# Kernel tuning notes

Measured on AMD Instinct MI355X. Metric: run time of the kernel, lower is better.

The kernel has to match this reference:

```python
import jax, jax.numpy as jnp
import numpy as np
from jax.ops import segment_sum

N_NODES = 50000
N_EDGES = 800000
HIDDEN = 96
N_CLASSES = 10
N_GRAPHS = 64


def gcn_conv(x, W, b, src, dst, num_nodes):
    """PyG GCNConv: symmetric-normalized aggregation with self-loops.
    out = D^{-1/2} (A + I) D^{-1/2} (x W) + b, with D the degree of A + I.
    Self-loop contribution handled analytically instead of appending edges.
    """
    ones = jnp.ones((src.shape[0],), dtype=x.dtype)
    deg = segment_sum(ones, dst, num_segments=num_nodes) + 1.0  # +1 for self-loop
    dinv = jax.lax.rsqrt(deg)
    h = x @ W  # [N, H] small GEMM
    norm = dinv[src] * dinv[dst]  # [E]
    msg = h[src] * norm[:, None]  # [E, H] dominant gather
    out = segment_sum(msg, dst, num_segments=num_nodes)  # scatter-add
    out = out + h * (dinv * dinv)[:, None]  # self-loop term
    return out + b


def setup_inputs() -> dict:
    key = jax.random.key(0)
    ks = jax.random.split(key, 12)
    x = jax.random.normal(ks[0], (N_NODES, HIDDEN), dtype=jnp.float32)
    edge_index = jax.random.randint(ks[1], (2, N_EDGES), 0, N_NODES, dtype=jnp.int64)
    batch = jnp.sort(jax.random.randint(ks[2], (N_NODES,), 0, N_GRAPHS, dtype=jnp.int64))
    s = 1.0 / np.sqrt(HIDDEN)
    W0 = jax.random.normal(ks[3], (HIDDEN, HIDDEN), dtype=jnp.float32) * s
    b0 = jnp.zeros((HIDDEN,), dtype=jnp.float32)
    W1 = jax.random.normal(ks[4], (HIDDEN, HIDDEN), dtype=jnp.float32) * s
    b1 = jnp.zeros((HIDDEN,), dtype=jnp.float32)
    W2 = jax.random.normal(ks[5], (HIDDEN, HIDDEN), dtype=jnp.float32) * s
    b2 = jnp.zeros((HIDDEN,), dtype=jnp.float32)
    W_lin = jax.random.normal(ks[6], (HIDDEN, N_CLASSES), dtype=jnp.float32) * s
    b_lin = jnp.zeros((N_CLASSES,), dtype=jnp.float32)
    return {"x": x, "edge_index": edge_index, "batch": batch,
            "W0": W0, "b0": b0, "W1": W1, "b1": b1, "W2": W2, "b2": b2,
            "W_lin": W_lin, "b_lin": b_lin}


def reference(x, edge_index, batch, W0, b0, W1, b1, W2, b2, W_lin, b_lin):
    src, dst = edge_index[0], edge_index[1]
    n = x.shape[0]
    h = jax.nn.relu(gcn_conv(x, W0, b0, src, dst, n))
    h = jax.nn.relu(gcn_conv(h, W1, b1, src, dst, n))
    h = gcn_conv(h, W2, b2, src, dst, n)  # last layer: no activation
    # global_mean_pool over batch index
    sums = segment_sum(h, batch, num_segments=N_GRAPHS)  # [G, H]
    cnts = segment_sum(jnp.ones((n,), dtype=h.dtype), batch, num_segments=N_GRAPHS)
    pooled = sums / jnp.maximum(cnts, 1.0)[:, None]
    # dropout is identity in eval mode
    return pooled @ W_lin + b_lin  # [G, num_classes]
```

## Files before the change

kernel.cpp:

```cpp
#include <hip/hip_runtime.h>
#include <hip/hip_bf16.h>

#define HID 96
#define NGRAPHS 64
#define SENT 0xC3C3u
#define NROWS 50116

typedef __attribute__((ext_vector_type(8))) short short8;
typedef __attribute__((ext_vector_type(4))) float floatx4;
typedef __attribute__((ext_vector_type(8))) unsigned short ushort8v;

__device__ __forceinline__ float bf16_to_f32(unsigned short u) {
    unsigned int v = ((unsigned int)u) << 16;
    return __builtin_bit_cast(float, v);
}
__device__ __forceinline__ unsigned short f32_to_bf16(float f) {
    unsigned int u = __builtin_bit_cast(unsigned int, f);
    u += 0x7fff + ((u >> 16) & 1);
    return (unsigned short)(u >> 16);
}

__device__ __forceinline__ void gather_batch(const unsigned short* __restrict__ h,
                                             const unsigned short* __restrict__ csr,
                                             int i, int fi, float& a0, float& a1) {
    ushort8v iv = *(const ushort8v*)(csr + i);
    ushort2 v0 = *(const ushort2*)(h + (size_t)iv[0] * HID + fi);
    ushort2 v1 = *(const ushort2*)(h + (size_t)iv[1] * HID + fi);
    ushort2 v2 = *(const ushort2*)(h + (size_t)iv[2] * HID + fi);
    ushort2 v3 = *(const ushort2*)(h + (size_t)iv[3] * HID + fi);
    ushort2 v4 = *(const ushort2*)(h + (size_t)iv[4] * HID + fi);
    ushort2 v5 = *(const ushort2*)(h + (size_t)iv[5] * HID + fi);
    ushort2 v6 = *(const ushort2*)(h + (size_t)iv[6] * HID + fi);
    ushort2 v7 = *(const ushort2*)(h + (size_t)iv[7] * HID + fi);
    a0 += bf16_to_f32(v0.x) + bf16_to_f32(v1.x) + bf16_to_f32(v2.x) +
          bf16_to_f32(v3.x) + bf16_to_f32(v4.x) + bf16_to_f32(v5.x) +
          bf16_to_f32(v6.x) + bf16_to_f32(v7.x);
    a1 += bf16_to_f32(v0.y) + bf16_to_f32(v1.y) + bf16_to_f32(v2.y) +
          bf16_to_f32(v3.y) + bf16_to_f32(v4.y) + bf16_to_f32(v5.y) +
          bf16_to_f32(v6.y) + bf16_to_f32(v7.y);
}

__device__ __forceinline__ void gather2(const unsigned short* __restrict__ h,
                                        const unsigned short* __restrict__ csr,
                                        int i0, int e0, int i1, int e1, int fi,
                                        float& a00, float& a01, float& a10,
                                        float& a11) {
    ushort8v ivA, ivB;
    if (i0 < e0) ivA = *(const ushort8v*)(csr + i0);
    if (i1 < e1) ivB = *(const ushort8v*)(csr + i1);
    while (i0 < e0 && i1 < e1) {
        ushort8v ca = ivA, cb = ivB;
        i0 += 8;
        i1 += 8;
        if (i0 < e0) ivA = *(const ushort8v*)(csr + i0);
        if (i1 < e1) ivB = *(const ushort8v*)(csr + i1);
        ushort2 u0 = *(const ushort2*)(h + (size_t)ca[0] * HID + fi);
        ushort2 u1 = *(const ushort2*)(h + (size_t)ca[1] * HID + fi);
        ushort2 u2 = *(const ushort2*)(h + (size_t)ca[2] * HID + fi);
        ushort2 u3 = *(const ushort2*)(h + (size_t)ca[3] * HID + fi);
        ushort2 u4 = *(const ushort2*)(h + (size_t)ca[4] * HID + fi);
        ushort2 u5 = *(const ushort2*)(h + (size_t)ca[5] * HID + fi);
        ushort2 u6 = *(const ushort2*)(h + (size_t)ca[6] * HID + fi);
        ushort2 u7 = *(const ushort2*)(h + (size_t)ca[7] * HID + fi);
        ushort2 w0 = *(const ushort2*)(h + (size_t)cb[0] * HID + fi);
        ushort2 w1 = *(const ushort2*)(h + (size_t)cb[1] * HID + fi);
        ushort2 w2 = *(const ushort2*)(h + (size_t)cb[2] * HID + fi);
        ushort2 w3 = *(const ushort2*)(h + (size_t)cb[3] * HID + fi);
        ushort2 w4 = *(const ushort2*)(h + (size_t)cb[4] * HID + fi);
        ushort2 w5 = *(const ushort2*)(h + (size_t)cb[5] * HID + fi);
        ushort2 w6 = *(const ushort2*)(h + (size_t)cb[6] * HID + fi);
        ushort2 w7 = *(const ushort2*)(h + (size_t)cb[7] * HID + fi);
        a00 += bf16_to_f32(u0.x) + bf16_to_f32(u1.x) + bf16_to_f32(u2.x) +
               bf16_to_f32(u3.x) + bf16_to_f32(u4.x) + bf16_to_f32(u5.x) +
               bf16_to_f32(u6.x) + bf16_to_f32(u7.x);
        a01 += bf16_to_f32(u0.y) + bf16_to_f32(u1.y) + bf16_to_f32(u2.y) +
               bf16_to_f32(u3.y) + bf16_to_f32(u4.y) + bf16_to_f32(u5.y) +
               bf16_to_f32(u6.y) + bf16_to_f32(u7.y);
        a10 += bf16_to_f32(w0.x) + bf16_to_f32(w1.x) + bf16_to_f32(w2.x) +
               bf16_to_f32(w3.x) + bf16_to_f32(w4.x) + bf16_to_f32(w5.x) +
               bf16_to_f32(w6.x) + bf16_to_f32(w7.x);
        a11 += bf16_to_f32(w0.y) + bf16_to_f32(w1.y) + bf16_to_f32(w2.y) +
               bf16_to_f32(w3.y) + bf16_to_f32(w4.y) + bf16_to_f32(w5.y) +
               bf16_to_f32(w6.y) + bf16_to_f32(w7.y);
    }
    for (; i0 < e0; i0 += 8) gather_batch(h, csr, i0, fi, a00, a01);
    for (; i1 < e1; i1 += 8) gather_batch(h, csr, i1, fi, a10, a11);
}

__global__ void deg_kernel(const int* __restrict__ dst, int* __restrict__ deg,
                           int n_edges) {
    int t = blockIdx.x * blockDim.x + threadIdx.x;
    int e0 = t * 4;
    if (e0 + 4 <= n_edges) {
        int4 d4 = *(const int4*)(dst + e0);
        atomicAdd(&deg[d4.x], 1);
        atomicAdd(&deg[d4.y], 1);
        atomicAdd(&deg[d4.z], 1);
        atomicAdd(&deg[d4.w], 1);
    } else {
        for (int e = e0; e < n_edges; e++) atomicAdd(&deg[dst[e]], 1);
    }
}

__global__ __launch_bounds__(256) void scan_phaseA(const int* __restrict__ deg,
                                                   float* __restrict__ dinv,
                                                   int* __restrict__ blocksum,
                                                   int N) {
    int i = blockIdx.x * 256 + threadIdx.x;
    int d = (i < N) ? deg[i] : 0;
    if (i < N) dinv[i] = rsqrtf((float)d + 1.0f);
    int v = (d + 7) & ~7;
#pragma unroll
    for (int off = 32; off > 0; off >>= 1) v += __shfl_down(v, off, 64);
    __shared__ int s[4];
    if ((threadIdx.x & 63) == 0) s[threadIdx.x >> 6] = v;
    __syncthreads();
    if (threadIdx.x == 0) blocksum[blockIdx.x] = s[0] + s[1] + s[2] + s[3];
}

__global__ __launch_bounds__(256) void scan_phaseB(int* __restrict__ blocksum,
                                                   int* __restrict__ blockoff,
                                                   int nblocks) {
    __shared__ int s[256];
    int t = threadIdx.x;
    int own = (t < nblocks) ? blocksum[t] : 0;
    s[t] = own;
    __syncthreads();
#pragma unroll
    for (int off = 1; off < 256; off <<= 1) {
        int v = (t >= off) ? s[t - off] : 0;
        __syncthreads();
        s[t] += v;
        __syncthreads();
    }
    if (t < nblocks) blockoff[t] = s[t] - own;
}

__global__ __launch_bounds__(256) void scan_phaseC(const int* __restrict__ deg,
                                                   const int* __restrict__ blockoff,
                                                   int* __restrict__ rowptr,
                                                   int* __restrict__ cursor, int N) {
    __shared__ int s[256];
    int t = threadIdx.x;
    int i = blockIdx.x * 256 + t;
    int own = (i < N) ? (deg[i] + 7) & ~7 : 0;
    s[t] = own;
    __syncthreads();
#pragma unroll
    for (int off = 1; off < 256; off <<= 1) {
        int v = (t >= off) ? s[t - off] : 0;
        __syncthreads();
        s[t] += v;
        __syncthreads();
    }
    if (i < N) {
        int r = blockoff[blockIdx.x] + s[t] - own;
        rowptr[i] = r;
        cursor[i] = r;
        if (i == N - 1) rowptr[N] = r + own;
    }
}

__global__ void csr_fill(const int* __restrict__ src, const int* __restrict__ dst,
                         int* __restrict__ cursor,
                         unsigned short* __restrict__ csr_src, int n_edges) {
    int t = blockIdx.x * blockDim.x + threadIdx.x;
    int e0 = t * 4;
    if (e0 + 4 <= n_edges) {
        int4 d4 = *(const int4*)(dst + e0);
        int4 s4 = *(const int4*)(src + e0);
        int p0 = atomicAdd(&cursor[d4.x], 1);
        int p1 = atomicAdd(&cursor[d4.y], 1);
        int p2 = atomicAdd(&cursor[d4.z], 1);
        int p3 = atomicAdd(&cursor[d4.w], 1);
        csr_src[p0] = (unsigned short)s4.x;
        csr_src[p1] = (unsigned short)s4.y;
        csr_src[p2] = (unsigned short)s4.z;
        csr_src[p3] = (unsigned short)s4.w;
    } else {
        for (int e = e0; e < n_edges; e++) {
            int p = atomicAdd(&cursor[dst[e]], 1);
            csr_src[p] = (unsigned short)src[e];
        }
    }
}

__global__ void swizzle_W(const float* __restrict__ W0, const float* __restrict__ W1,
                          const float* __restrict__ W2, unsigned short* __restrict__ Wz) {
    const float* W = (blockIdx.x == 0) ? W0 : (blockIdx.x == 1) ? W1 : W2;
    unsigned short* dst = Wz + blockIdx.x * HID * HID;
    for (int e = threadIdx.x; e < HID * HID; e += blockDim.x) {
        int k = e / HID, n = e % HID;
        int nt = n >> 4, kki = k >> 5, quad = (k >> 3) & 3, j = k & 7;
        int lane = (n & 15) | (quad << 4);
        dst[(((nt * 3 + kki) * 64 + lane) << 3) | j] = f32_to_bf16(W[e]);
    }
}

__global__ void zero_sentinel(unsigned short* __restrict__ a,
                              unsigned short* __restrict__ b) {
    int t = threadIdx.x;
    a[(size_t)SENT * HID + t] = 0;
    b[(size_t)SENT * HID + t] = 0;
}

__global__ __launch_bounds__(256) void gemm0_f32(
    const float* __restrict__ X, const unsigned short* __restrict__ Wz,
    const float* __restrict__ dinv, unsigned short* __restrict__ Out, int Mtiles) {
    int wv = threadIdx.x >> 6;
    int lane = threadIdx.x & 63;
    int quad = lane >> 4;
    int mrow = lane & 15;
    int tt = blockIdx.x * 2 + (wv >> 1);
    int half = wv & 1;
    if (tt >= Mtiles) return;

    short8 bfrag[9];
    const short8* Wz8 = (const short8*)Wz;
#pragma unroll
    for (int f = 0; f < 9; f++) bfrag[f] = Wz8[(half * 9 + f) * 64 + lane];

    int m0 = tt * 16;
    const float* arow = X + (size_t)(m0 + mrow) * HID + quad * 8;
    short8 a[3];
#pragma unroll
    for (int kb = 0; kb < 3; kb++) {
        float4 u = *(const float4*)(arow + kb * 32);
        float4 v = *(const float4*)(arow + kb * 32 + 4);
        short8 t;
        t[0] = (short)f32_to_bf16(u.x); t[1] = (short)f32_to_bf16(u.y);
        t[2] = (short)f32_to_bf16(u.z); t[3] = (short)f32_to_bf16(u.w);
        t[4] = (short)f32_to_bf16(v.x); t[5] = (short)f32_to_bf16(v.y);
        t[6] = (short)f32_to_bf16(v.z); t[7] = (short)f32_to_bf16(v.w);
        a[kb] = t;
    }
    float dscale[4];
#pragma unroll
    for (int r = 0; r < 4; r++) dscale[r] = dinv[m0 + quad * 4 + r];
    unsigned short* orow = Out + (size_t)m0 * HID;
#pragma unroll
    for (int ntl = 0; ntl < 3; ntl++) {
        int nt = half * 3 + ntl;
        floatx4 c = {0.0f, 0.0f, 0.0f, 0.0f};
        c = __builtin_amdgcn_mfma_f32_16x16x32_bf16(a[0], bfrag[ntl * 3 + 0], c, 0, 0, 0);
        c = __builtin_amdgcn_mfma_f32_16x16x32_bf16(a[1], bfrag[ntl * 3 + 1], c, 0, 0, 0);
        c = __builtin_amdgcn_mfma_f32_16x16x32_bf16(a[2], bfrag[ntl * 3 + 2], c, 0, 0, 0);
#pragma unroll
        for (int r = 0; r < 4; r++)
            orow[(size_t)(quad * 4 + r) * HID + nt * 16 + mrow] =
                f32_to_bf16(c[r] * dscale[r]);
    }
}

__global__ __launch_bounds__(256) void fused_gather_gemm(
    const unsigned short* __restrict__ h, const int* __restrict__ rowptr,
    const unsigned short* __restrict__ csr, const float* __restrict__ dinv,
    const float* __restrict__ bias, const unsigned short* __restrict__ Wz,
    unsigned short* __restrict__ Out, int Mtiles) {
    __shared__ unsigned short tile[2][16][104];
    int wv = threadIdx.x >> 6;
    int lane = threadIdx.x & 63;
    int quad = lane >> 4;
    int mrow = lane & 15;
    int tsel = wv >> 1;
    int half = wv & 1;
    int tt = blockIdx.x * 2 + tsel;
    bool active = tt < Mtiles;
    int fi = (lane < 48) ? lane * 2 : 94;

    if (active) {
        float b0 = bias[fi], b1 = bias[fi + 1];
        int n0 = tt * 16;
        for (int jj = 0; jj < 8; jj += 2) {
            int j0 = half * 8 + jj;
            int na = n0 + j0;
            int nb = na + 1;
            int ia = rowptr[na];
            int ea = rowptr[na + 1];
            int ib = ea;
            int eb = rowptr[nb + 1];
            float da = dinv[na], db = dinv[nb];
            ushort2 ha = *(const ushort2*)(h + (size_t)na * HID + fi);
            ushort2 hb = *(const ushort2*)(h + (size_t)nb * HID + fi);
            float a00 = bf16_to_f32(ha.x), a01 = bf16_to_f32(ha.y);
            float a10 = bf16_to_f32(hb.x), a11 = bf16_to_f32(hb.y);
            gather2(h, csr, ia, ea, ib, eb, fi, a00, a01, a10, a11);
            a00 = fmaxf(a00 * da + b0, 0.0f);
            a01 = fmaxf(a01 * da + b1, 0.0f);
            a10 = fmaxf(a10 * db + b0, 0.0f);
            a11 = fmaxf(a11 * db + b1, 0.0f);
            if (lane < 48) {
                tile[tsel][j0][fi] = f32_to_bf16(a00);
                tile[tsel][j0][fi + 1] = f32_to_bf16(a01);
                tile[tsel][j0 + 1][fi] = f32_to_bf16(a10);
                tile[tsel][j0 + 1][fi + 1] = f32_to_bf16(a11);
            }
        }
    }
    __syncthreads();
    if (!active) return;

    short8 bfrag[9];
    const short8* Wz8 = (const short8*)Wz;
#pragma unroll
    for (int f = 0; f < 9; f++) bfrag[f] = Wz8[(half * 9 + f) * 64 + lane];

    const unsigned short* tp = &tile[tsel][0][0];
    short8 a[3];
#pragma unroll
    for (int kb = 0; kb < 3; kb++)
        a[kb] = *(const short8*)(tp + mrow * 104 + quad * 8 + kb * 32);
    int n0 = tt * 16;
    float dscale[4];
#pragma unroll
    for (int r = 0; r < 4; r++) dscale[r] = dinv[n0 + quad * 4 + r];
    unsigned short* orow = Out + (size_t)n0 * HID;
#pragma unroll
    for (int ntl = 0; ntl < 3; ntl++) {
        int nt = half * 3 + ntl;
        floatx4 c = {0.0f, 0.0f, 0.0f, 0.0f};
        c = __builtin_amdgcn_mfma_f32_16x16x32_bf16(a[0], bfrag[ntl * 3 + 0], c, 0, 0, 0);
        c = __builtin_amdgcn_mfma_f32_16x16x32_bf16(a[1], bfrag[ntl * 3 + 1], c, 0, 0, 0);
        c = __builtin_amdgcn_mfma_f32_16x16x32_bf16(a[2], bfrag[ntl * 3 + 2], c, 0, 0, 0);
#pragma unroll
        for (int r = 0; r < 4; r++)
            orow[(size_t)(quad * 4 + r) * HID + nt * 16 + mrow] =
                f32_to_bf16(c[r] * dscale[r]);
    }
}

__global__ __launch_bounds__(256) void gather_pool(
    const unsigned short* __restrict__ h, const int* __restrict__ rowptr,
    const unsigned short* __restrict__ csr, const float* __restrict__ dinv,
    const float* __restrict__ bias, const int* __restrict__ batch,
    float* __restrict__ psum, float* __restrict__ pcnt, int Ntiles8) {
    int wv = threadIdx.x >> 6;
    int lane = threadIdx.x & 63;
    int tt = blockIdx.x * 4 + wv;
    if (tt >= Ntiles8) return;
    int fi = (lane < 48) ? lane * 2 : 94;
    float b0 = bias[fi], b1 = bias[fi + 1];

    int n0 = tt * 8;
    int g_cur = batch[n0];
    float s0 = 0.0f, s1 = 0.0f;
    int cnt = 0;
    for (int jj = 0; jj < 8; jj += 2) {
        int na = n0 + jj;
        int nb = na + 1;
        int ia = rowptr[na];
        int ea = rowptr[na + 1];
        int ib = ea;
        int eb = rowptr[nb + 1];
        float da = dinv[na], db = dinv[nb];
        ushort2 ha = *(const ushort2*)(h + (size_t)na * HID + fi);
        ushort2 hb = *(const ushort2*)(h + (size_t)nb * HID + fi);
        float a00 = bf16_to_f32(ha.x), a01 = bf16_to_f32(ha.y);
        float a10 = bf16_to_f32(hb.x), a11 = bf16_to_f32(hb.y);
        gather2(h, csr, ia, ea, ib, eb, fi, a00, a01, a10, a11);
        a00 = a00 * da + b0;
        a01 = a01 * da + b1;
        a10 = a10 * db + b0;
        a11 = a11 * db + b1;
        int ga = batch[na];
        if (ga != g_cur) {
            if (lane < 48) {
                atomicAdd(&psum[g_cur * HID + fi], s0);
                atomicAdd(&psum[g_cur * HID + fi + 1], s1);
            }
            if (lane == 0) atomicAdd(&pcnt[g_cur], (float)cnt);
            s0 = 0.0f; s1 = 0.0f; cnt = 0;
            g_cur = ga;
        }
        s0 += a00; s1 += a01; cnt++;
        int gb = batch[nb];
        if (gb != g_cur) {
            if (lane < 48) {
                atomicAdd(&psum[g_cur * HID + fi], s0);
                atomicAdd(&psum[g_cur * HID + fi + 1], s1);
            }
            if (lane == 0) atomicAdd(&pcnt[g_cur], (float)cnt);
            s0 = 0.0f; s1 = 0.0f; cnt = 0;
            g_cur = gb;
        }
        s0 += a10; s1 += a11; cnt++;
    }
    if (lane < 48) {
        atomicAdd(&psum[g_cur * HID + fi], s0);
        atomicAdd(&psum[g_cur * HID + fi + 1], s1);
    }
    if (lane == 0) atomicAdd(&pcnt[g_cur], (float)cnt);
}

__global__ __launch_bounds__(640) void final_kernel(
    const float* __restrict__ sums, const float* __restrict__ cnts,
    const float* __restrict__ Wlin, const float* __restrict__ blin,
    float* __restrict__ out) {
    int t = threadIdx.x;
    if (t >= NGRAPHS * 10) return;
    int g = t / 10;
    int c = t % 10;
    float denom = fmaxf(cnts[g], 1.0f);
    float acc = blin[c];
#pragma unroll
    for (int f = 0; f < HID; f++)
        acc += (sums[g * HID + f] / denom) * Wlin[f * 10 + c];
    out[t] = acc;
}

extern "C" void kernel_launch(void* const* d_in, const int* in_sizes, int n_in,
                              void* d_out, int out_size, void* d_ws,
                              size_t ws_size, hipStream_t stream) {
    const float* x = (const float*)d_in[0];
    const int* edge = (const int*)d_in[1];
    const int* batch = (const int*)d_in[2];
    const float* W[3] = {(const float*)d_in[3], (const float*)d_in[5],
                         (const float*)d_in[7]};
    const float* B[3] = {(const float*)d_in[4], (const float*)d_in[6],
                         (const float*)d_in[8]};
    const float* Wlin = (const float*)d_in[9];
    const float* blin = (const float*)d_in[10];
    float* out = (float*)d_out;

    int N = in_sizes[0] / HID;
    int E = in_sizes[1] / 2;
    const int* src = edge;
    const int* dst = edge + E;
    int NB = (N + 255) / 256;

    char* ws = (char*)d_ws;
    size_t off = 0;
    auto alloc = [&](size_t bytes) {
        void* p = ws + off;
        off += (bytes + 255) & ~(size_t)255;
        return p;
    };
    int* deg = (int*)alloc((size_t)N * 4);
    float* dinv = (float*)alloc((size_t)N * 4);
    int* rowptr = (int*)alloc(((size_t)N + 1) * 4);
    int* cursor = (int*)alloc((size_t)N * 4);
    int* blocksum = (int*)alloc((size_t)NB * 4);
    int* blockoff = (int*)alloc((size_t)NB * 4);
    size_t csr_cap = (size_t)E + 8 * (size_t)N;
    unsigned short* csr_src = (unsigned short*)alloc(csr_cap * 2 + 64);
    unsigned short* Wz = (unsigned short*)alloc(3 * HID * HID * 2);
    unsigned short* bufA = (unsigned short*)alloc((size_t)NROWS * HID * 2);
    unsigned short* bufB = (unsigned short*)alloc((size_t)NROWS * HID * 2);
    float* psum = (float*)alloc((NGRAPHS * HID + NGRAPHS) * 4);
    float* pcnt = psum + NGRAPHS * HID;

    hipMemsetAsync(deg, 0, (size_t)N * 4, stream);
    hipMemsetAsync(csr_src, 0xC3, csr_cap * 2, stream);
    hipMemsetAsync(psum, 0, (NGRAPHS * HID + NGRAPHS) * 4, stream);
    deg_kernel<<<(E / 4 + 255) / 256, 256, 0, stream>>>(dst, deg, E);
    scan_phaseA<<<NB, 256, 0, stream>>>(deg, dinv, blocksum, N);
    scan_phaseB<<<1, 256, 0, stream>>>(blocksum, blockoff, NB);
    scan_phaseC<<<NB, 256, 0, stream>>>(deg, blockoff, rowptr, cursor, N);
    csr_fill<<<(E / 4 + 255) / 256, 256, 0, stream>>>(src, dst, cursor, csr_src, E);
    swizzle_W<<<3, 256, 0, stream>>>(W[0], W[1], W[2], Wz);
    zero_sentinel<<<1, HID, 0, stream>>>(bufA, bufB);

    int Mtiles = (N + 15) / 16;
    int grid2 = (Mtiles + 1) / 2;
    int Ntiles8 = (N + 7) / 8;
    int gridp = (Ntiles8 + 3) / 4;

    gemm0_f32<<<grid2, 256, 0, stream>>>(x, Wz, dinv, bufA, Mtiles);
    fused_gather_gemm<<<grid2, 256, 0, stream>>>(
        bufA, rowptr, csr_src, dinv, B[0], Wz + 1 * HID * HID, bufB, Mtiles);
    fused_gather_gemm<<<grid2, 256, 0, stream>>>(
        bufB, rowptr, csr_src, dinv, B[1], Wz + 2 * HID * HID, bufA, Mtiles);
    gather_pool<<<gridp, 256, 0, stream>>>(bufA, rowptr, csr_src, dinv, B[2],
                                           batch, psum, pcnt, Ntiles8);
    final_kernel<<<1, 640, 0, stream>>>(psum, pcnt, Wlin, blin, out);
}
```

Before: 319.8 us.

## Merge setup kernels, fold scan phase B, shrink gather tiles, drop index prefetch

Replaces two memsets and the sentinel zeroing with a single init kernel, and folds the single-block scan phase into phase C by having each block reduce its preceding block sums. csr_fill now handles 8 edges per thread. fused_gather_gemm runs one 16-row tile per 128-thread block instead of two tiles per 256 threads, and gather_pool handles 4 nodes per wave instead of 8, giving more blocks to spread gather load. The software prefetch of CSR index vectors in gather2 is removed, which simplifies the loop but may expose index load latency.

After: 358.4 us. +12.1%, slower.

```diff
diff --git a/kernel.cpp b/kernel.cpp
--- a/kernel.cpp
+++ b/kernel.cpp
@@ -45,15 +45,11 @@
                                         int i0, int e0, int i1, int e1, int fi,
                                         float& a00, float& a01, float& a10,
                                         float& a11) {
-    ushort8v ivA, ivB;
-    if (i0 < e0) ivA = *(const ushort8v*)(csr + i0);
-    if (i1 < e1) ivB = *(const ushort8v*)(csr + i1);
     while (i0 < e0 && i1 < e1) {
-        ushort8v ca = ivA, cb = ivB;
+        ushort8v ca = *(const ushort8v*)(csr + i0);
+        ushort8v cb = *(const ushort8v*)(csr + i1);
         i0 += 8;
         i1 += 8;
-        if (i0 < e0) ivA = *(const ushort8v*)(csr + i0);
-        if (i1 < e1) ivB = *(const ushort8v*)(csr + i1);
         ushort2 u0 = *(const ushort2*)(h + (size_t)ca[0] * HID + fi);
         ushort2 u1 = *(const ushort2*)(h + (size_t)ca[1] * HID + fi);
         ushort2 u2 = *(const ushort2*)(h + (size_t)ca[2] * HID + fi);
@@ -87,6 +83,18 @@
     for (; i1 < e1; i1 += 8) gather_batch(h, csr, i1, fi, a10, a11);
 }
 
+__global__ __launch_bounds__(256) void init_kernel(
+    int* __restrict__ deg, float* __restrict__ psum,
+    unsigned short* __restrict__ bufA, unsigned short* __restrict__ bufB, int N) {
+    int i = blockIdx.x * 256 + threadIdx.x;
+    if (i < N) deg[i] = 0;
+    if (i < NGRAPHS * HID + NGRAPHS) psum[i] = 0.0f;
+    if (i < HID) {
+        bufA[(size_t)SENT * HID + i] = 0;
+        bufB[(size_t)SENT * HID + i] = 0;
+    }
+}
+
 __global__ void deg_kernel(const int* __restrict__ dst, int* __restrict__ deg,
                            int n_edges) {
     int t = blockIdx.x * blockDim.x + threadIdx.x;
@@ -118,12 +126,23 @@
     if (threadIdx.x == 0) blocksum[blockIdx.x] = s[0] + s[1] + s[2] + s[3];
 }
 
-__global__ __launch_bounds__(256) void scan_phaseB(int* __restrict__ blocksum,
-                                                   int* __restrict__ blockoff,
-                                                   int nblocks) {
+__global__ __launch_bounds__(256) void scan_phaseC(const int* __restrict__ deg,
+                                                   const int* __restrict__ blocksum,
+                                                   int* __restrict__ rowptr,
+                                                   int* __restrict__ cursor,
+                                                   int N, int NB) {
+    int t = threadIdx.x;
+    int mine = (t < NB && t < blockIdx.x) ? blocksum[t] : 0;
+#pragma unroll
+    for (int off = 32; off > 0; off >>= 1) mine += __shfl_down(mine, off, 64);
+    __shared__ int ps[4];
+    if ((t & 63) == 0) ps[t >> 6] = mine;
+    __syncthreads();
+    int pref = ps[0] + ps[1] + ps[2] + ps[3];
+
     __shared__ int s[256];
-    int t = threadIdx.x;
-    int own = (t < nblocks) ? blocksum[t] : 0;
+    int i = blockIdx.x * 256 + t;
+    int own = (i < N) ? (deg[i] + 7) & ~7 : 0;
     s[t] = own;
     __syncthreads();
 #pragma unroll
@@ -133,28 +152,8 @@
         s[t] += v;
         __syncthreads();
     }
-    if (t < nblocks) blockoff[t] = s[t] - own;
-}
-
-__global__ __launch_bounds__(256) void scan_phaseC(const int* __restrict__ deg,
-                                                   const int* __restrict__ blockoff,
-                                                   int* __restrict__ rowptr,
-                                                   int* __restrict__ cursor, int N) {
-    __shared__ int s[256];
-    int t = threadIdx.x;
-    int i = blockIdx.x * 256 + t;
-    int own = (i < N) ? (deg[i] + 7) & ~7 : 0;
-    s[t] = own;
-    __syncthreads();
-#pragma unroll
-    for (int off = 1; off < 256; off <<= 1) {
-        int v = (t >= off) ? s[t - off] : 0;
-        __syncthreads();
-        s[t] += v;
-        __syncthreads();
-    }
     if (i < N) {
-        int r = blockoff[blockIdx.x] + s[t] - own;
+        int r = pref + s[t] - own;
         rowptr[i] = r;
         cursor[i] = r;
         if (i == N - 1) rowptr[N] = r + own;
@@ -165,18 +164,28 @@
                          int* __restrict__ cursor,
                          unsigned short* __restrict__ csr_src, int n_edges) {
     int t = blockIdx.x * blockDim.x + threadIdx.x;
-    int e0 = t * 4;
-    if (e0 + 4 <= n_edges) {
-        int4 d4 = *(const int4*)(dst + e0);
-        int4 s4 = *(const int4*)(src + e0);
-        int p0 = atomicAdd(&cursor[d4.x], 1);
-        int p1 = atomicAdd(&cursor[d4.y], 1);
-        int p2 = atomicAdd(&cursor[d4.z], 1);
-        int p3 = atomicAdd(&cursor[d4.w], 1);
-        csr_src[p0] = (unsigned short)s4.x;
-        csr_src[p1] = (unsigned short)s4.y;
-        csr_src[p2] = (unsigned short)s4.z;
-        csr_src[p3] = (unsigned short)s4.w;
+    int e0 = t * 8;
+    if (e0 + 8 <= n_edges) {
+        int4 da = *(const int4*)(dst + e0);
+        int4 db = *(const int4*)(dst + e0 + 4);
+        int4 sa = *(const int4*)(src + e0);
+        int4 sb = *(const int4*)(src + e0 + 4);
+        int p0 = atomicAdd(&cursor[da.x], 1);
+        int p1 = atomicAdd(&cursor[da.y], 1);
+        int p2 = atomicAdd(&cursor[da.z], 1);
+        int p3 = atomicAdd(&cursor[da.w], 1);
+        int p4 = atomicAdd(&cursor[db.x], 1);
+        int p5 = atomicAdd(&cursor[db.y], 1);
+        int p6 = atomicAdd(&cursor[db.z], 1);
+        int p7 = atomicAdd(&cursor[db.w], 1);
+        csr_src[p0] = (unsigned short)sa.x;
+        csr_src[p1] = (unsigned short)sa.y;
+        csr_src[p2] = (unsigned short)sa.z;
+        csr_src[p3] = (unsigned short)sa.w;
+        csr_src[p4] = (unsigned short)sb.x;
+        csr_src[p5] = (unsigned short)sb.y;
+        csr_src[p6] = (unsigned short)sb.z;
+        csr_src[p7] = (unsigned short)sb.w;
     } else {
         for (int e = e0; e < n_edges; e++) {
             int p = atomicAdd(&cursor[dst[e]], 1);
@@ -195,13 +204,6 @@
         int lane = (n & 15) | (quad << 4);
         dst[(((nt * 3 + kki) * 64 + lane) << 3) | j] = f32_to_bf16(W[e]);
     }
-}
-
-__global__ void zero_sentinel(unsigned short* __restrict__ a,
-                              unsigned short* __restrict__ b) {
-    int t = threadIdx.x;
-    a[(size_t)SENT * HID + t] = 0;
-    b[(size_t)SENT * HID + t] = 0;
 }
 
 __global__ __launch_bounds__(256) void gemm0_f32(
@@ -252,23 +254,20 @@
     }
 }
 
-__global__ __launch_bounds__(256) void fused_gather_gemm(
+__global__ __launch_bounds__(128) void fused_gather_gemm(
     const unsigned short* __restrict__ h, const int* __restrict__ rowptr,
     const unsigned short* __restrict__ csr, const float* __restrict__ dinv,
     const float* __restrict__ bias, const unsigned short* __restrict__ Wz,
     unsigned short* __restrict__ Out, int Mtiles) {
-    __shared__ unsigned short tile[2][16][104];
-    int wv = threadIdx.x >> 6;
+    __shared__ unsigned short tile[16][104];
+    int half = threadIdx.x >> 6;
     int lane = threadIdx.x & 63;
     int quad = lane >> 4;
     int mrow = lane & 15;
-    int tsel = wv >> 1;
-    int half = wv & 1;
-    int tt = blockIdx.x * 2 + tsel;
-    bool active = tt < Mtiles;
+    int tt = blockIdx.x;
     int fi = (lane < 48) ? lane * 2 : 94;
 
-    if (active) {
+    {
         float b0 = bias[fi], b1 = bias[fi + 1];
         int n0 = tt * 16;
         for (int jj = 0; jj < 8; jj += 2) {
@@ -290,22 +289,21 @@
             a10 = fmaxf(a10 * db + b0, 0.0f);
             a11 = fmaxf(a11 * db + b1, 0.0f);
             if (lane < 48) {
-                tile[tsel][j0][fi] = f32_to_bf16(a00);
-                tile[tsel][j0][fi + 1] = f32_to_bf16(a01);
-                tile[tsel][j0 + 1][fi] = f32_to_bf16(a10);
-                tile[tsel][j0 + 1][fi + 1] = f32_to_bf16(a11);
+                tile[j0][fi] = f32_to_bf16(a00);
+                tile[j0][fi + 1] = f32_to_bf16(a01);
+                tile[j0 + 1][fi] = f32_to_bf16(a10);
+                tile[j0 + 1][fi + 1] = f32_to_bf16(a11);
             }
         }
     }
     __syncthreads();
-    if (!active) return;
 
     short8 bfrag[9];
     const short8* Wz8 = (const short8*)Wz;
 #pragma unroll
     for (int f = 0; f < 9; f++) bfrag[f] = Wz8[(half * 9 + f) * 64 + lane];
 
-    const unsigned short* tp = &tile[tsel][0][0];
+    const unsigned short* tp = &tile[0][0];
     short8 a[3];
 #pragma unroll
     for (int kb = 0; kb < 3; kb++)
@@ -333,19 +331,19 @@
     const unsigned short* __restrict__ h, const int* __restrict__ rowptr,
     const unsigned short* __restrict__ csr, const float* __restrict__ dinv,
     const float* __restrict__ bias, const int* __restrict__ batch,
-    float* __restrict__ psum, float* __restrict__ pcnt, int Ntiles8) {
+    float* __restrict__ psum, float* __restrict__ pcnt, int Ntiles4) {
     int wv = threadIdx.x >> 6;
     int lane = threadIdx.x & 63;
     int tt = blockIdx.x * 4 + wv;
-    if (tt >= Ntiles8) return;
+    if (tt >= Ntiles4) return;
     int fi = (lane < 48) ? lane * 2 : 94;
     float b0 = bias[fi], b1 = bias[fi + 1];
 
-    int n0 = tt * 8;
+    int n0 = tt * 4;
     int g_cur = batch[n0];
     float s0 = 0.0f, s1 = 0.0f;
     int cnt = 0;
-    for (int jj = 0; jj < 8; jj += 2) {
+    for (int jj = 0; jj < 4; jj += 2) {
         int na = n0 + jj;
         int nb = na + 1;
         int ia = rowptr[na];
@@ -440,7 +438,6 @@
     int* rowptr = (int*)alloc(((size_t)N + 1) * 4);
     int* cursor = (int*)alloc((size_t)N * 4);
     int* blocksum = (int*)alloc((size_t)NB * 4);
-    int* blockoff = (int*)alloc((size_t)NB * 4);
     size_t csr_cap = (size_t)E + 8 * (size_t)N;
     unsigned short* csr_src = (unsigned short*)alloc(csr_cap * 2 + 64);
     unsigned short* Wz = (unsigned short*)alloc(3 * HID * HID * 2);
@@ -449,28 +446,25 @@
     float* psum = (float*)alloc((NGRAPHS * HID + NGRAPHS) * 4);
     float* pcnt = psum + NGRAPHS * HID;
 
-    hipMemsetAsync(deg, 0, (size_t)N * 4, stream);
     hipMemsetAsync(csr_src, 0xC3, csr_cap * 2, stream);
-    hipMemsetAsync(psum, 0, (NGRAPHS * HID + NGRAPHS) * 4, stream);
+    init_kernel<<<NB, 256, 0, stream>>>(deg, psum, bufA, bufB, N);
     deg_kernel<<<(E / 4 + 255) / 256, 256, 0, stream>>>(dst, deg, E);
     scan_phaseA<<<NB, 256, 0, stream>>>(deg, dinv, blocksum, N);
-    scan_phaseB<<<1, 256, 0, stream>>>(blocksum, blockoff, NB);
-    scan_phaseC<<<NB, 256, 0, stream>>>(deg, blockoff, rowptr, cursor, N);
-    csr_fill<<<(E / 4 + 255) / 256, 256, 0, stream>>>(src, dst, cursor, csr_src, E);
+    scan_phaseC<<<NB, 256, 0, stream>>>(deg, blocksum, rowptr, cursor, N, NB);
+    csr_fill<<<(E / 8 + 255) / 256, 256, 0, stream>>>(src, dst, cursor, csr_src, E);
     swizzle_W<<<3, 256, 0, stream>>>(W[0], W[1], W[2], Wz);
-    zero_sentinel<<<1, HID, 0, stream>>>(bufA, bufB);
 
     int Mtiles = (N + 15) / 16;
     int grid2 = (Mtiles + 1) / 2;
-    int Ntiles8 = (N + 7) / 8;
-    int gridp = (Ntiles8 + 3) / 4;
+    int Ntiles4 = (N + 3) / 4;
+    int gridp = (Ntiles4 + 3) / 4;
 
     gemm0_f32<<<grid2, 256, 0, stream>>>(x, Wz, dinv, bufA, Mtiles);
-    fused_gather_gemm<<<grid2, 256, 0, stream>>>(
+    fused_gather_gemm<<<Mtiles, 128, 0, stream>>>(
         bufA, rowptr, csr_src, dinv, B[0], Wz + 1 * HID * HID, bufB, Mtiles);
-    fused_gather_gemm<<<grid2, 256, 0, stream>>>(
+    fused_gather_gemm<<<Mtiles, 128, 0, stream>>>(
         bufB, rowptr, csr_src, dinv, B[1], Wz + 2 * HID * HID, bufA, Mtiles);
     gather_pool<<<gridp, 256, 0, stream>>>(bufA, rowptr, csr_src, dinv, B[2],
-                                           batch, psum, pcnt, Ntiles8);
+                                           batch, psum, pcnt, Ntiles4);
     final_kernel<<<1, 640, 0, stream>>>(psum, pcnt, Wlin, blin, out);
 }
```
